# Performance work log

Measured on AMD Instinct MI355X. Metric: run time of the kernel, lower is better.

The kernel has to match this reference:

```python
import jax, jax.numpy as jnp
import numpy as np

N = 100000
E = 3200000
F_IN = 128
H1, H2 = 32, 16
R = 8
G = 512  # number of graphs in batch


def setup_inputs() -> dict:
    key = jax.random.key(0)
    ks = jax.random.split(key, 12)
    x = jax.random.normal(ks[0], (N, F_IN), dtype=jnp.float32)
    edge_index = jax.random.randint(ks[1], (2, E), 0, N, dtype=jnp.int64)
    edge_attr = jax.random.randint(ks[2], (E,), 0, R, dtype=jnp.int64)
    batch = jnp.sort(jax.random.randint(ks[3], (N,), 0, G, dtype=jnp.int64))
    s1 = 1.0 / np.sqrt(F_IN)
    s2 = 1.0 / np.sqrt(H1)
    s3 = 1.0 / np.sqrt(H2)
    W1 = jax.random.uniform(ks[4], (R, F_IN, H1), jnp.float32, -s1, s1)
    root1 = jax.random.uniform(ks[5], (F_IN, H1), jnp.float32, -s1, s1)
    b1 = jnp.zeros((H1,), jnp.float32)
    W2 = jax.random.uniform(ks[6], (R, H1, H2), jnp.float32, -s2, s2)
    root2 = jax.random.uniform(ks[7], (H1, H2), jnp.float32, -s2, s2)
    b2 = jnp.zeros((H2,), jnp.float32)
    dense_w = jax.random.uniform(ks[8], (H2, 1), jnp.float32, -s3, s3)
    dense_b = jax.random.uniform(ks[9], (1,), jnp.float32, -s3, s3)
    return dict(x=x, edge_index=edge_index, edge_attr=edge_attr, batch=batch,
                W1=W1, root1=root1, b1=b1, W2=W2, root2=root2, b2=b2,
                dense_w=dense_w, dense_b=dense_b)


def rgcn_layer(x, W, root, b, src, dst, rel, num_rel):
    # Per-relation transform of all nodes: [N, R, out]
    xw = jnp.einsum('ni,rio->nro', x, W)
    msgs = xw[src, rel]                      # gather per edge: [E, out]
    seg = dst * num_rel + rel                # (node, relation) segment id
    nr = x.shape[0] * num_rel
    sums = jax.ops.segment_sum(msgs, seg, num_segments=nr)
    cnt = jax.ops.segment_sum(jnp.ones(src.shape, x.dtype), seg, num_segments=nr)
    mean = sums / jnp.maximum(cnt, 1.0)[:, None]
    agg = mean.reshape(x.shape[0], num_rel, -1).sum(axis=1)  # sum over relations
    return agg + x @ root + b


def reference(x, edge_index, edge_attr, batch, W1, root1, b1, W2, root2, b2, dense_w, dense_b):
    src, dst = edge_index[0], edge_index[1]
    rel = edge_attr
    h = jax.nn.relu(rgcn_layer(x, W1, root1, b1, src, dst, rel, R))
    # F.dropout is treated as identity (inference) for a deterministic reference
    h = jax.nn.relu(rgcn_layer(h, W2, root2, b2, src, dst, rel, R))
    pooled = jax.ops.segment_max(h, batch, num_segments=G)
    pooled = jnp.where(jnp.isfinite(pooled), pooled, 0.0)  # empty graphs -> 0
    return pooled @ dense_w + dense_b
```

## Files before the change

### kernel.cpp

```cpp
#include <hip/hip_runtime.h>
#include <hip/hip_bf16.h>

#define RNUM 8
#define HH1 32
#define HH2 16
#define FIN 128
#define BNODES 256
#define NBMAX 512
#define PCHUNK 8192
#define SORTCAP 11264

#define W1STR 136
#define W1ELTS (288 * W1STR)
#define W2STR 40
#define W2ELTS (144 * W2STR)

typedef short bf16x8 __attribute__((ext_vector_type(8)));
typedef float f32x4 __attribute__((ext_vector_type(4)));

__device__ inline bf16x8 cvt8(const float* __restrict__ p) {
  float tmp[8];
  *(float4*)tmp = *(const float4*)p;
  *(float4*)(tmp + 4) = *(const float4*)(p + 4);
  bf16x8 r;
  #pragma unroll
  for (int j = 0; j < 8; ++j) {
    union { __hip_bfloat16 h; short s; } cv;
    cv.h = __float2bfloat16(tmp[j]);
    r[j] = cv.s;
  }
  return r;
}

__device__ inline bf16x8 cvt8relu(const float* __restrict__ p) {
  float tmp[8];
  *(float4*)tmp = *(const float4*)p;
  *(float4*)(tmp + 4) = *(const float4*)(p + 4);
  bf16x8 r;
  #pragma unroll
  for (int j = 0; j < 8; ++j) {
    union { __hip_bfloat16 h; short s; } cv;
    cv.h = __float2bfloat16(fmaxf(tmp[j], 0.f));
    r[j] = cv.s;
  }
  return r;
}

__global__ __launch_bounds__(256) void k_bhist(const int* __restrict__ ei,
    int* __restrict__ ghist, int E, int NB) {
  __shared__ int h[NBMAX];
  int t = threadIdx.x;
  for (int i = t; i < NBMAX; i += 256) h[i] = 0;
  __syncthreads();
  int base = blockIdx.x * 4096;
  #pragma unroll
  for (int j = 0; j < 16; ++j) {
    int e = base + j * 256 + t;
    if (e < E) atomicAdd(&h[ei[E + e] >> 8], 1);
  }
  __syncthreads();
  for (int i = t; i < NB; i += 256)
    if (h[i]) atomicAdd(&ghist[i], h[i]);
}

__global__ __launch_bounds__(NBMAX) void k_bscan(const int* __restrict__ ghist,
    int* __restrict__ bbase, int* __restrict__ gcursor, int NB, int E) {
  __shared__ int buf[NBMAX];
  int t = threadIdx.x;
  int v = (t < NB) ? ghist[t] : 0;
  buf[t] = v;
  __syncthreads();
  for (int d = 1; d < NBMAX; d <<= 1) {
    int w = (t >= d) ? buf[t - d] : 0;
    __syncthreads();
    buf[t] += w;
    __syncthreads();
  }
  if (t < NB) {
    int ex = buf[t] - v;
    bbase[t] = ex;
    gcursor[t] = ex;
  }
  if (t == 0) bbase[NB] = E;
}

__global__ __launch_bounds__(512) void k_part(const int* __restrict__ ei,
    const int* __restrict__ ea, int* __restrict__ gcursor,
    unsigned* __restrict__ ebuf, int E, int NB) {
  __shared__ unsigned reorder[PCHUNK];
  __shared__ unsigned short bkt[PCHUNK];
  __shared__ int hist[NBMAX], startl[NBMAX], cursor[NBMAX], gb[NBMAX], scanb[NBMAX];
  int t = threadIdx.x;
  int base = blockIdx.x * PCHUNK;
  int cn = min(PCHUNK, E - base);
  unsigned key[16];
  short bb[16];
  hist[t] = 0;
  __syncthreads();
  #pragma unroll
  for (int j = 0; j < 16; ++j) {
    int e = base + j * 512 + t;
    bb[j] = -1;
    if (e < E) {
      int src = ei[e], dst = ei[E + e], rel = ea[e];
      key[j] = ((unsigned)(dst & (BNODES - 1)) << 20) | ((unsigned)src << 3) | (unsigned)rel;
      int b = dst >> 8;
      bb[j] = (short)b;
      atomicAdd(&hist[b], 1);
    }
  }
  __syncthreads();
  int v = hist[t];
  scanb[t] = v;
  __syncthreads();
  for (int d = 1; d < NBMAX; d <<= 1) {
    int w = (t >= d) ? scanb[t - d] : 0;
    __syncthreads();
    scanb[t] += w;
    __syncthreads();
  }
  startl[t] = scanb[t] - v;
  cursor[t] = scanb[t] - v;
  __syncthreads();
  #pragma unroll
  for (int j = 0; j < 16; ++j) {
    if (bb[j] >= 0) {
      int pos = atomicAdd(&cursor[bb[j]], 1);
      reorder[pos] = key[j];
      bkt[pos] = (unsigned short)bb[j];
    }
  }
  __syncthreads();
  if (t < NB && hist[t] > 0) gb[t] = atomicAdd(&gcursor[t], hist[t]);
  __syncthreads();
  for (int p = t; p < cn; p += 512) {
    int b = bkt[p];
    ebuf[gb[b] + (p - startl[b])] = reorder[p];
  }
}

__global__ __launch_bounds__(512) void k_sort(const int* __restrict__ bbase,
    const unsigned* __restrict__ ebuf, unsigned* __restrict__ ebuf2,
    float* __restrict__ wbuf, int* __restrict__ rps, int* __restrict__ rpc,
    int NB) {
  __shared__ int hist[2048];
  __shared__ float invw[2048];
  __shared__ int dlc[256];
  __shared__ unsigned sorted[SORTCAP];
  int t = threadIdx.x;
  int b = blockIdx.x;
  int s = bbase[b], e = bbase[b + 1];
  int out_s = ((s + 7) & ~7) + (b << 11);
  for (int i = t; i < 2048; i += 512) hist[i] = 0;
  __syncthreads();
  for (int p = s + t; p < e; p += 512) {
    unsigned k = ebuf[p];
    atomicAdd(&hist[((k >> 20) << 3) | (k & 7u)], 1);
  }
  __syncthreads();
  for (int i = t; i < 2048; i += 512) {
    int c = hist[i];
    invw[i] = 1.0f / (float)(c > 1 ? c : 1);
  }
  __syncthreads();
  int pr[8];
  int cdl = 0, pc = 0;
  if (t < 256) {
    #pragma unroll
    for (int r = 0; r < 8; ++r) { pr[r] = cdl; cdl += hist[8 * t + r]; }
    pc = (cdl + 7) & ~7;
    dlc[t] = pc;
  }
  __syncthreads();
  for (int d = 1; d < 256; d <<= 1) {
    int w = (t < 256 && t >= d) ? dlc[t - d] : 0;
    __syncthreads();
    if (t < 256) dlc[t] += w;
    __syncthreads();
  }
  if (t < 256) {
    int ebase = dlc[t] - pc;
    #pragma unroll
    for (int r = 0; r < 8; ++r) hist[8 * t + r] = ebase + pr[r];
    rps[(b << 8) + t] = out_s + ebase;
    rpc[(b << 8) + t] = cdl;
  }
  __syncthreads();
  int ptot = dlc[255];
  if (ptot <= SORTCAP) {
    for (int p = t; p < ptot; p += 512) sorted[p] = 0xFFFFFFFFu;
    __syncthreads();
    for (int p = s + t; p < e; p += 512) {
      unsigned k = ebuf[p];
      int pos = atomicAdd(&hist[((k >> 20) << 3) | (k & 7u)], 1);
      sorted[pos] = k;
    }
    __syncthreads();
    for (int p = t; p < ptot; p += 512) {
      unsigned k = sorted[p];
      int o = out_s + p;
      if (k == 0xFFFFFFFFu) { ebuf2[o] = 0u; wbuf[o] = 0.f; }
      else { ebuf2[o] = k; wbuf[o] = invw[((k >> 20) << 3) | (k & 7u)]; }
    }
  } else {
    if (t < 256) {
      int ebase = dlc[t] - pc;
      for (int p = ebase + cdl; p < dlc[t]; ++p) {
        ebuf2[out_s + p] = 0u; wbuf[out_s + p] = 0.f;
      }
    }
    __syncthreads();
    for (int p = s + t; p < e; p += 512) {
      unsigned k = ebuf[p];
      int bin = ((k >> 20) << 3) | (k & 7u);
      int pos = atomicAdd(&hist[bin], 1);
      ebuf2[out_s + pos] = k;
      wbuf[out_s + pos] = invw[bin];
    }
  }
}

__global__ __launch_bounds__(256) void k_prepw(const float* __restrict__ W1,
    const float* __restrict__ root1, const float* __restrict__ W2,
    const float* __restrict__ root2, unsigned short* __restrict__ Wcat,
    unsigned short* __restrict__ W2cat) {
  int id = blockIdx.x * 256 + threadIdx.x;
  union { __hip_bfloat16 h; unsigned short u; } cv;
  if (id < W1ELTS) {
    int c = id / W1STR, kk = id - c * W1STR;
    float v = 0.f;
    if (kk < FIN)
      v = (c < 256) ? W1[((size_t)(c >> 5) * FIN + kk) * HH1 + (c & 31)]
                    : root1[(size_t)kk * HH1 + (c - 256)];
    cv.h = __float2bfloat16(v);
    Wcat[id] = cv.u;
  } else if (id < W1ELTS + W2ELTS) {
    int id2 = id - W1ELTS;
    int c = id2 / W2STR, kk = id2 - c * W2STR;
    float v = 0.f;
    if (kk < HH1)
      v = (c < 128) ? W2[((size_t)(c >> 4) * HH1 + kk) * HH2 + (c & 15)]
                    : root2[(size_t)kk * HH2 + (c - 128)];
    cv.h = __float2bfloat16(v);
    W2cat[id2] = cv.u;
  }
}

__global__ __launch_bounds__(384) void k_gemm1m(const float* __restrict__ x,
    const unsigned short* __restrict__ Wcat, const float* __restrict__ b1,
    __hip_bfloat16* __restrict__ xw, float* __restrict__ agg, int N) {
  int lane = threadIdx.x & 63;
  int wv = threadIdx.x >> 6;
  int g = lane >> 4, lc = lane & 15;
  int cj0 = wv * 3;
  bf16x8 B[3][4];
  #pragma unroll
  for (int j = 0; j < 3; ++j)
    #pragma unroll
    for (int ks = 0; ks < 4; ++ks)
      B[j][ks] = *(const bf16x8*)(Wcat + (size_t)((cj0 + j) * 16 + lc) * W1STR + ks * 32 + g * 8);

  #pragma unroll
  for (int tt = 0; tt < 2; ++tt) {
    long base = ((long)blockIdx.x * 2 + tt) * 64;
    if (base >= N) break;
    f32x4 acc[4][3];
    #pragma unroll
    for (int rf = 0; rf < 4; ++rf)
      #pragma unroll
      for (int j = 0; j < 3; ++j)
        acc[rf][j] = (f32x4){0.f, 0.f, 0.f, 0.f};
    #pragma unroll
    for (int rf = 0; rf < 4; ++rf) {
      long row = base + rf * 16 + lc;
      if (row > N - 1) row = N - 1;
      bf16x8 a[4];
      #pragma unroll
      for (int ks = 0; ks < 4; ++ks)
        a[ks] = cvt8(x + row * FIN + ks * 32 + g * 8);
      #pragma unroll
      for (int j = 0; j < 3; ++j)
        #pragma unroll
        for (int ks = 0; ks < 4; ++ks)
          acc[rf][j] = __builtin_amdgcn_mfma_f32_16x16x32_bf16(a[ks], B[j][ks], acc[rf][j], 0, 0, 0);
    }
    #pragma unroll
    for (int rf = 0; rf < 4; ++rf) {
      #pragma unroll
      for (int j = 0; j < 3; ++j) {
        int col = (cj0 + j) * 16 + lc;
        #pragma unroll
        for (int q = 0; q < 4; ++q) {
          long row = base + rf * 16 + g * 4 + q;
          if (row < N) {
            if (col < 256) {
              xw[row * 256 + col] = __float2bfloat16(acc[rf][j][q]);
            } else {
              agg[row * HH1 + (col - 256)] = acc[rf][j][q] + b1[col - 256];
            }
          }
        }
      }
    }
  }
}

__global__ __launch_bounds__(256) void k_agg1(const int* __restrict__ rps,
    const int* __restrict__ rpc, const unsigned* __restrict__ eb,
    const float* __restrict__ wb, const __hip_bfloat16* __restrict__ xw,
    float* __restrict__ agg, int N) {
  int d = blockIdx.x * 4 + (threadIdx.x >> 6);
  if (d >= N) return;
  int lane = threadIdx.x & 63;
  int h = lane & 31, half = lane >> 5;
  int s = rps[d];
  int cnt = rpc[d];
  float acc = 0.f;
  for (int j = half * 8; j < cnt; j += 16) {
    const unsigned* kp = eb + s + j;
    uint4 ka = *(const uint4*)kp;
    uint4 kb = *(const uint4*)(kp + 4);
    float4 wa = *(const float4*)(wb + s + j);
    float4 wc = *(const float4*)(wb + s + j + 4);
    unsigned ks[8] = {ka.x, ka.y, ka.z, ka.w, kb.x, kb.y, kb.z, kb.w};
    float ws[8] = {wa.x, wa.y, wa.z, wa.w, wc.x, wc.y, wc.z, wc.w};
    #pragma unroll
    for (int u = 0; u < 8; ++u) {
      unsigned idx = ks[u] & 0xFFFFFu;
      float v = __bfloat162float(xw[((size_t)idx << 5) + h]);
      acc = fmaf(ws[u], v, acc);
    }
  }
  acc += __shfl_xor(acc, 32);
  if (half == 0) agg[((size_t)d << 5) + h] += acc;
}

__global__ __launch_bounds__(256) void k_gemm2m(const float* __restrict__ agg1,
    const unsigned short* __restrict__ W2cat, const float* __restrict__ b2,
    __hip_bfloat16* __restrict__ xw, float* __restrict__ agg, int N) {
  __shared__ short WL[W2ELTS];
  int t = threadIdx.x;
  for (int i = t; i < W2ELTS / 8; i += 256)
    ((uint4*)WL)[i] = ((const uint4*)W2cat)[i];
  __syncthreads();
  int lane = t & 63;
  int wv = t >> 6;
  int g = lane >> 4, lc = lane & 15;
  long nb = (long)blockIdx.x * 128 + wv * 32;
  f32x4 acc[2][9];
  #pragma unroll
  for (int m = 0; m < 2; ++m)
    #pragma unroll
    for (int j = 0; j < 9; ++j)
      acc[m][j] = (f32x4){0.f, 0.f, 0.f, 0.f};
  long rowA0 = nb + lc;       if (rowA0 > N - 1) rowA0 = N - 1;
  long rowA1 = nb + 16 + lc;  if (rowA1 > N - 1) rowA1 = N - 1;
  bf16x8 a0 = cvt8relu(agg1 + rowA0 * HH1 + g * 8);
  bf16x8 a1 = cvt8relu(agg1 + rowA1 * HH1 + g * 8);
  #pragma unroll
  for (int j = 0; j < 9; ++j) {
    bf16x8 bf = *(const bf16x8*)(WL + (16 * j + lc) * W2STR + g * 8);
    acc[0][j] = __builtin_amdgcn_mfma_f32_16x16x32_bf16(a0, bf, acc[0][j], 0, 0, 0);
    acc[1][j] = __builtin_amdgcn_mfma_f32_16x16x32_bf16(a1, bf, acc[1][j], 0, 0, 0);
  }
  #pragma unroll
  for (int m = 0; m < 2; ++m) {
    #pragma unroll
    for (int j = 0; j < 9; ++j) {
      #pragma unroll
      for (int q = 0; q < 4; ++q) {
        long row = nb + 16 * m + g * 4 + q;
        if (row < N) {
          if (j < 8) {
            xw[row * 128 + 16 * j + lc] = __float2bfloat16(acc[m][j][q]);
          } else {
            agg[row * HH2 + lc] = acc[m][j][q] + b2[lc];
          }
        }
      }
    }
  }
}

__global__ __launch_bounds__(256) void k_agg2(const int* __restrict__ rps,
    const int* __restrict__ rpc, const unsigned* __restrict__ eb,
    const float* __restrict__ wb, const __hip_bfloat16* __restrict__ xw,
    float* __restrict__ agg, int N) {
  int d = blockIdx.x * 4 + (threadIdx.x >> 6);
  if (d >= N) return;
  int lane = threadIdx.x & 63;
  int h = lane & 15, q = lane >> 4;
  int s = rps[d];
  int cnt = rpc[d];
  float acc = 0.f;
  for (int j = q * 8; j < cnt; j += 32) {
    const unsigned* kp = eb + s + j;
    uint4 ka = *(const uint4*)kp;
    uint4 kb = *(const uint4*)(kp + 4);
    float4 wa = *(const float4*)(wb + s + j);
    float4 wc = *(const float4*)(wb + s + j + 4);
    unsigned ks[8] = {ka.x, ka.y, ka.z, ka.w, kb.x, kb.y, kb.z, kb.w};
    float ws[8] = {wa.x, wa.y, wa.z, wa.w, wc.x, wc.y, wc.z, wc.w};
    #pragma unroll
    for (int u = 0; u < 8; ++u) {
      unsigned idx = ks[u] & 0xFFFFFu;
      float v = __bfloat162float(xw[((size_t)idx << 4) + h]);
      acc = fmaf(ws[u], v, acc);
    }
  }
  acc += __shfl_xor(acc, 32);
  acc += __shfl_xor(acc, 16);
  if (q == 0) agg[((size_t)d << 4) + h] += acc;
}

__global__ __launch_bounds__(256) void k_pool(const float* __restrict__ agg2,
    const int* __restrict__ batch, unsigned* __restrict__ pooled, int N) {
  int gid = blockIdx.x * 256 + threadIdx.x;
  int n = gid >> 4;
  if (n < N) {
    int h = gid & 15;
    float v = fmaxf(agg2[(size_t)n * HH2 + h], 0.f);
    atomicMax(&pooled[batch[n] * HH2 + h], __float_as_uint(v));
  }
}

__global__ __launch_bounds__(256) void k_dense(const float* __restrict__ pooled,
    const float* __restrict__ dw, const float* __restrict__ db,
    float* __restrict__ out, int Gn) {
  int g = blockIdx.x * 256 + threadIdx.x;
  if (g < Gn) {
    float s = db[0];
    #pragma unroll
    for (int h = 0; h < HH2; ++h) s += pooled[(size_t)g * HH2 + h] * dw[h];
    out[g] = s;
  }
}

extern "C" void kernel_launch(void* const* d_in, const int* in_sizes, int n_in,
                              void* d_out, int out_size, void* d_ws, size_t ws_size,
                              hipStream_t stream) {
  const float* x     = (const float*)d_in[0];
  const int*   ei    = (const int*)d_in[1];
  const int*   ea    = (const int*)d_in[2];
  const int*   batch = (const int*)d_in[3];
  const float* W1    = (const float*)d_in[4];
  const float* root1 = (const float*)d_in[5];
  const float* b1    = (const float*)d_in[6];
  const float* W2    = (const float*)d_in[7];
  const float* root2 = (const float*)d_in[8];
  const float* b2    = (const float*)d_in[9];
  const float* dw    = (const float*)d_in[10];
  const float* db    = (const float*)d_in[11];
  float* out = (float*)d_out;

  const int N  = in_sizes[0] / FIN;
  const int E  = in_sizes[2];
  const int Gn = out_size;
  const int NB = (N + BNODES - 1) / BNODES;

  char* ws = (char*)d_ws;
  size_t off = 0;
  auto walloc = [&](size_t bytes) -> void* {
    void* p = (void*)(ws + off);
    off += (bytes + 255) & ~(size_t)255;
    return p;
  };
  const size_t EP = (size_t)E + (size_t)NBMAX * 2048 + 64;
  int*            ghist   = (int*)            walloc((size_t)NBMAX * 4);
  int*            bbase   = (int*)            walloc(((size_t)NBMAX + 1) * 4);
  int*            gcursor = (int*)            walloc((size_t)NBMAX * 4);
  unsigned*       ebuf    = (unsigned*)       walloc((size_t)E * 4);
  unsigned*       ebuf2   = (unsigned*)       walloc(EP * 4);
  float*          wbuf    = (float*)          walloc(EP * 4);
  int*            rps     = (int*)            walloc((size_t)NBMAX * 256 * 4);
  int*            rpc     = (int*)            walloc((size_t)NBMAX * 256 * 4);
  unsigned short* Wcat    = (unsigned short*) walloc((size_t)W1ELTS * 2);
  unsigned short* W2cat   = (unsigned short*) walloc((size_t)W2ELTS * 2);
  __hip_bfloat16* xw1     = (__hip_bfloat16*) walloc((size_t)N * RNUM * HH1 * 2);
  float*          agg1    = (float*)          walloc((size_t)N * HH1 * 4);
  __hip_bfloat16* xw2     = (__hip_bfloat16*) walloc((size_t)N * RNUM * HH2 * 2);
  float*          agg2    = (float*)          walloc((size_t)N * HH2 * 4);
  unsigned*       pooled  = (unsigned*)       walloc((size_t)Gn * HH2 * 4);

  hipMemsetAsync(ghist, 0, (size_t)NBMAX * 4, stream);
  hipMemsetAsync(pooled, 0, (size_t)Gn * HH2 * 4, stream);

  k_prepw<<<(W1ELTS + W2ELTS + 255) / 256, 256, 0, stream>>>(W1, root1, W2, root2, Wcat, W2cat);
  k_bhist<<<(E + 4095) / 4096, 256, 0, stream>>>(ei, ghist, E, NB);
  k_bscan<<<1, NBMAX, 0, stream>>>(ghist, bbase, gcursor, NB, E);
  k_part<<<(E + PCHUNK - 1) / PCHUNK, 512, 0, stream>>>(ei, ea, gcursor, ebuf, E, NB);
  k_sort<<<NB, 512, 0, stream>>>(bbase, ebuf, ebuf2, wbuf, rps, rpc, NB);

  k_gemm1m<<<(N + 127) / 128, 384, 0, stream>>>(x, Wcat, b1, xw1, agg1, N);
  k_agg1<<<(N + 3) / 4, 256, 0, stream>>>(rps, rpc, ebuf2, wbuf, xw1, agg1, N);
  k_gemm2m<<<(N + 127) / 128, 256, 0, stream>>>(agg1, W2cat, b2, xw2, agg2, N);
  k_agg2<<<(N + 3) / 4, 256, 0, stream>>>(rps, rpc, ebuf2, wbuf, xw2, agg2, N);
  k_pool<<<(int)(((long)N * HH2 + 255) / 256), 256, 0, stream>>>(agg2, batch, pooled, N);
  k_dense<<<(Gn + 255) / 256, 256, 0, stream>>>((const float*)pooled, dw, db, out, Gn);
}
```

Baseline: 318.6 us.

## Swap MFMA operands to get row-contiguous outputs and vectorize GEMM stores

Both GEMM kernels swap the A/B operands of the MFMA so each lane holds four consecutive output columns of one row. This lets results go out as packed 4×bf16 (8-byte) and float4 stores instead of scattered 2-byte and 4-byte stores. The first GEMM also becomes a persistent grid-stride kernel over 32-row chunks, capped at 512 blocks, so its weight fragments are loaded once per block. The aim is to cut store transaction count and weight reloads. In exchange, the first GEMM has fewer rows in flight per iteration and depends on the chunk loop to hide latency.

```diff
diff --git a/kernel.cpp b/kernel.cpp
--- a/kernel.cpp
+++ b/kernel.cpp
@@ -44,6 +44,16 @@
     r[j] = cv.s;
   }
   return r;
+}
+
+__device__ inline uint2 pack4bf(f32x4 v) {
+  union { unsigned short u[4]; uint2 w; } pk;
+  union { __hip_bfloat16 h; unsigned short s; } cv;
+  cv.h = __float2bfloat16(v[0]); pk.u[0] = cv.s;
+  cv.h = __float2bfloat16(v[1]); pk.u[1] = cv.s;
+  cv.h = __float2bfloat16(v[2]); pk.u[2] = cv.s;
+  cv.h = __float2bfloat16(v[3]); pk.u[3] = cv.s;
+  return pk.w;
 }
 
 __global__ __launch_bounds__(256) void k_bhist(const int* __restrict__ ei,
@@ -248,57 +258,67 @@
 
 __global__ __launch_bounds__(384) void k_gemm1m(const float* __restrict__ x,
     const unsigned short* __restrict__ Wcat, const float* __restrict__ b1,
-    __hip_bfloat16* __restrict__ xw, float* __restrict__ agg, int N) {
+    __hip_bfloat16* __restrict__ xw, float* __restrict__ agg, int N, int nchunk) {
   int lane = threadIdx.x & 63;
   int wv = threadIdx.x >> 6;
   int g = lane >> 4, lc = lane & 15;
   int cj0 = wv * 3;
-  bf16x8 B[3][4];
+  bf16x8 Wf[3][4];
   #pragma unroll
   for (int j = 0; j < 3; ++j)
     #pragma unroll
     for (int ks = 0; ks < 4; ++ks)
-      B[j][ks] = *(const bf16x8*)(Wcat + (size_t)((cj0 + j) * 16 + lc) * W1STR + ks * 32 + g * 8);
-
-  #pragma unroll
-  for (int tt = 0; tt < 2; ++tt) {
-    long base = ((long)blockIdx.x * 2 + tt) * 64;
-    if (base >= N) break;
-    f32x4 acc[4][3];
-    #pragma unroll
-    for (int rf = 0; rf < 4; ++rf)
+      Wf[j][ks] = *(const bf16x8*)(Wcat + (size_t)((cj0 + j) * 16 + lc) * W1STR + ks * 32 + g * 8);
+
+  for (int ch = blockIdx.x; ch < nchunk; ch += gridDim.x) {
+    long base = (long)ch * 32;
+    long r0 = base + lc;       if (r0 > N - 1) r0 = N - 1;
+    long r1 = base + 16 + lc;  if (r1 > N - 1) r1 = N - 1;
+    bf16x8 xf0[4], xf1[4];
+    #pragma unroll
+    for (int ks = 0; ks < 4; ++ks) xf0[ks] = cvt8(x + r0 * FIN + ks * 32 + g * 8);
+    #pragma unroll
+    for (int ks = 0; ks < 4; ++ks) xf1[ks] = cvt8(x + r1 * FIN + ks * 32 + g * 8);
+    f32x4 acc0[3], acc1[3];
+    #pragma unroll
+    for (int j = 0; j < 3; ++j) {
+      acc0[j] = (f32x4){0.f, 0.f, 0.f, 0.f};
+      acc1[j] = (f32x4){0.f, 0.f, 0.f, 0.f};
+    }
+    #pragma unroll
+    for (int j = 0; j < 3; ++j)
       #pragma unroll
-      for (int j = 0; j < 3; ++j)
-        acc[rf][j] = (f32x4){0.f, 0.f, 0.f, 0.f};
-    #pragma unroll
-    for (int rf = 0; rf < 4; ++rf) {
-      long row = base + rf * 16 + lc;
-      if (row > N - 1) row = N - 1;
-      bf16x8 a[4];
-      #pragma unroll
-      for (int ks = 0; ks < 4; ++ks)
-        a[ks] = cvt8(x + row * FIN + ks * 32 + g * 8);
-      #pragma unroll
-      for (int j = 0; j < 3; ++j)
-        #pragma unroll
-        for (int ks = 0; ks < 4; ++ks)
-          acc[rf][j] = __builtin_amdgcn_mfma_f32_16x16x32_bf16(a[ks], B[j][ks], acc[rf][j], 0, 0, 0);
-    }
-    #pragma unroll
-    for (int rf = 0; rf < 4; ++rf) {
+      for (int ks = 0; ks < 4; ++ks) {
+        acc0[j] = __builtin_amdgcn_mfma_f32_16x16x32_bf16(Wf[j][ks], xf0[ks], acc0[j], 0, 0, 0);
+        acc1[j] = __builtin_amdgcn_mfma_f32_16x16x32_bf16(Wf[j][ks], xf1[ks], acc1[j], 0, 0, 0);
+      }
+    long row0 = base + lc;
+    if (row0 < N) {
       #pragma unroll
       for (int j = 0; j < 3; ++j) {
-        int col = (cj0 + j) * 16 + lc;
-        #pragma unroll
-        for (int q = 0; q < 4; ++q) {
-          long row = base + rf * 16 + g * 4 + q;
-          if (row < N) {
-            if (col < 256) {
-              xw[row * 256 + col] = __float2bfloat16(acc[rf][j][q]);
-            } else {
-              agg[row * HH1 + (col - 256)] = acc[rf][j][q] + b1[col - 256];
-            }
-          }
+        int c0 = (cj0 + j) * 16 + 4 * g;
+        if (c0 < 256) {
+          *(uint2*)((unsigned short*)xw + row0 * 256 + c0) = pack4bf(acc0[j]);
+        } else {
+          float4 bb = *(const float4*)(b1 + (c0 - 256));
+          float4 o = make_float4(acc0[j][0] + bb.x, acc0[j][1] + bb.y,
+                                 acc0[j][2] + bb.z, acc0[j][3] + bb.w);
+          *(float4*)(agg + row0 * HH1 + (c0 - 256)) = o;
+        }
+      }
+    }
+    long row1 = base + 16 + lc;
+    if (row1 < N) {
+      #pragma unroll
+      for (int j = 0; j < 3; ++j) {
+        int c0 = (cj0 + j) * 16 + 4 * g;
+        if (c0 < 256) {
+          *(uint2*)((unsigned short*)xw + row1 * 256 + c0) = pack4bf(acc1[j]);
+        } else {
+          float4 bb = *(const float4*)(b1 + (c0 - 256));
+          float4 o = make_float4(acc1[j][0] + bb.x, acc1[j][1] + bb.y,
+                                 acc1[j][2] + bb.z, acc1[j][3] + bb.w);
+          *(float4*)(agg + row1 * HH1 + (c0 - 256)) = o;
         }
       }
     }
@@ -360,24 +380,20 @@
   #pragma unroll
   for (int j = 0; j < 9; ++j) {
     bf16x8 bf = *(const bf16x8*)(WL + (16 * j + lc) * W2STR + g * 8);
-    acc[0][j] = __builtin_amdgcn_mfma_f32_16x16x32_bf16(a0, bf, acc[0][j], 0, 0, 0);
-    acc[1][j] = __builtin_amdgcn_mfma_f32_16x16x32_bf16(a1, bf, acc[1][j], 0, 0, 0);
+    acc[0][j] = __builtin_amdgcn_mfma_f32_16x16x32_bf16(bf, a0, acc[0][j], 0, 0, 0);
+    acc[1][j] = __builtin_amdgcn_mfma_f32_16x16x32_bf16(bf, a1, acc[1][j], 0, 0, 0);
   }
   #pragma unroll
   for (int m = 0; m < 2; ++m) {
-    #pragma unroll
-    for (int j = 0; j < 9; ++j) {
+    long row = nb + 16 * m + lc;
+    if (row < N) {
       #pragma unroll
-      for (int q = 0; q < 4; ++q) {
-        long row = nb + 16 * m + g * 4 + q;
-        if (row < N) {
-          if (j < 8) {
-            xw[row * 128 + 16 * j + lc] = __float2bfloat16(acc[m][j][q]);
-          } else {
-            agg[row * HH2 + lc] = acc[m][j][q] + b2[lc];
-          }
-        }
-      }
+      for (int j = 0; j < 8; ++j)
+        *(uint2*)((unsigned short*)xw + row * 128 + 16 * j + 4 * g) = pack4bf(acc[m][j]);
+      float4 bb = *(const float4*)(b2 + 4 * g);
+      float4 o = make_float4(acc[m][8][0] + bb.x, acc[m][8][1] + bb.y,
+                             acc[m][8][2] + bb.z, acc[m][8][3] + bb.w);
+      *(float4*)(agg + row * HH2 + 4 * g) = o;
     }
   }
 }
@@ -491,7 +507,11 @@
   k_part<<<(E + PCHUNK - 1) / PCHUNK, 512, 0, stream>>>(ei, ea, gcursor, ebuf, E, NB);
   k_sort<<<NB, 512, 0, stream>>>(bbase, ebuf, ebuf2, wbuf, rps, rpc, NB);
 
-  k_gemm1m<<<(N + 127) / 128, 384, 0, stream>>>(x, Wcat, b1, xw1, agg1, N);
+  {
+    int nchunk = (N + 31) / 32;
+    int g1 = nchunk < 512 ? nchunk : 512;
+    k_gemm1m<<<g1, 384, 0, stream>>>(x, Wcat, b1, xw1, agg1, N, nchunk);
+  }
   k_agg1<<<(N + 3) / 4, 256, 0, stream>>>(rps, rpc, ebuf2, wbuf, xw1, agg1, N);
   k_gemm2m<<<(N + 127) / 128, 256, 0, stream>>>(agg1, W2cat, b2, xw2, agg2, N);
   k_agg2<<<(N + 3) / 4, 256, 0, stream>>>(rps, rpc, ebuf2, wbuf, xw2, agg2, N);
```

New measurement: 297.3 us. 1.07x faster.
